# Optimization experiments

Measured on AMD Instinct MI355X. Metric: run time of the kernel, lower is better.

Reference implementation:

```python
import jax, jax.numpy as jnp
import numpy as np

N, E, F, H, A, C, NC, L, AH = 50000, 800000, 768, 256, 128, 128, 7, 2, 4

def _ln(x, g, b):
    m = jnp.mean(x, axis=-1, keepdims=True)
    v = jnp.var(x, axis=-1, keepdims=True)
    return (x - m) / jnp.sqrt(v + 1e-5) * g + b

def setup_inputs() -> dict:
    key = jax.random.key(0)
    ks = jax.random.split(key, 32)
    s = 0.02
    d = {}
    d['x'] = jax.random.normal(ks[0], (N, F), jnp.float32)
    d['edge_index'] = jax.random.randint(ks[1], (2, E), 0, N, jnp.int32)
    d['W_in'] = jax.random.normal(ks[2], (F, H), jnp.float32) * s
    d['b_in'] = jnp.zeros((H,), jnp.float32)
    d['gin_W1'] = jax.random.normal(ks[3], (L, H, H), jnp.float32) * s
    d['gin_b1'] = jnp.zeros((L, H), jnp.float32)
    d['gin_lng'] = jnp.ones((L, H), jnp.float32)
    d['gin_lnb'] = jnp.zeros((L, H), jnp.float32)
    d['gin_W2'] = jax.random.normal(ks[4], (L, H, H), jnp.float32) * s
    d['gin_b2'] = jnp.zeros((L, H), jnp.float32)
    d['eps'] = jnp.zeros((L,), jnp.float32)
    d['ln_g'] = jnp.ones((L, H), jnp.float32)
    d['ln_b'] = jnp.zeros((L, H), jnp.float32)
    d['att_W1'] = jax.random.normal(ks[5], (AH, H, A), jnp.float32) * s
    d['att_b1'] = jnp.zeros((AH, A), jnp.float32)
    d['att_W2'] = jax.random.normal(ks[6], (AH, A), jnp.float32) * s
    d['att_b2'] = jnp.zeros((AH,), jnp.float32)
    d['Wc1'] = jax.random.normal(ks[7], (H, C), jnp.float32) * s
    d['bc1'] = jnp.zeros((C,), jnp.float32)
    d['lnc1_g'] = jnp.ones((C,), jnp.float32)
    d['lnc1_b'] = jnp.zeros((C,), jnp.float32)
    d['Wc2'] = jax.random.normal(ks[8], (C, C // 2), jnp.float32) * s
    d['bc2'] = jnp.zeros((C // 2,), jnp.float32)
    d['lnc2_g'] = jnp.ones((C // 2,), jnp.float32)
    d['lnc2_b'] = jnp.zeros((C // 2,), jnp.float32)
    d['Wc3'] = jax.random.normal(ks[9], (C // 2, NC), jnp.float32) * s
    d['bc3'] = jnp.zeros((NC,), jnp.float32)
    return d

def reference(x, edge_index, W_in, b_in, gin_W1, gin_b1, gin_lng, gin_lnb, gin_W2, gin_b2, eps, ln_g, ln_b, att_W1, att_b1, att_W2, att_b2, Wc1, bc1, lnc1_g, lnc1_b, Wc2, bc2, lnc2_g, lnc2_b, Wc3, bc3):
    src, dst = edge_index[0], edge_index[1]
    # input projection (use_residual and input_dim != gnn_hidden)
    h = x @ W_in + b_in  # [N,H]
    for i in range(L):
        agg = jax.ops.segment_sum(h[src], dst, num_segments=N)  # GIN sum aggregation
        m = (1.0 + eps[i]) * h + agg
        m = _ln(m @ gin_W1[i] + gin_b1[i], gin_lng[i], gin_lnb[i])
        m = jax.nn.relu(m) @ gin_W2[i] + gin_b2[i]
        hn = jax.nn.relu(_ln(m, ln_g[i], ln_b[i]))
        h = hn + h  # residual (shapes match)
    # multi-head attention pooling, softmax over node dim
    s = jnp.tanh(jnp.einsum('nd,kda->kna', h, att_W1) + att_b1[:, None, :])  # [AH,N,A]
    logits = jnp.einsum('kna,ka->kn', s, att_W2) + att_b2[:, None]  # [AH,N]
    a = jax.nn.softmax(logits, axis=1)  # [AH,N]
    z = jnp.einsum('kn,nd->kd', a, h)  # [AH,H]
    z_agg = jnp.mean(z, axis=0)  # [H]
    attn = a.T  # [N,AH]
    # classifier (full variant)
    c = jax.nn.relu(_ln(z_agg @ Wc1 + bc1, lnc1_g, lnc1_b))
    c = jax.nn.relu(_ln(c @ Wc2 + bc2, lnc2_g, lnc2_b))
    probs = jax.nn.softmax(c @ Wc3 + bc3, axis=0)
    return probs, attn
```

## Files before the change

### kernel.cpp

```cpp
#include <hip/hip_runtime.h>
#include <math.h>

#define NN 50000
#define NE 800000
#define FF 768
#define HH 256

typedef __attribute__((ext_vector_type(8))) short short8;
typedef __attribute__((ext_vector_type(4))) float f32x4;

__device__ inline unsigned short f2bf(float f) {
  unsigned u = __float_as_uint(f);
  u = u + 0x7fffu + ((u >> 16) & 1u);
  return (unsigned short)(u >> 16);
}
__device__ inline float bf2f(unsigned short b) {
  return __uint_as_float(((unsigned)b) << 16);
}

__device__ __forceinline__ void ldsload16(const unsigned short* g, unsigned short* l) {
  __builtin_amdgcn_global_load_lds(
      (const __attribute__((address_space(1))) void*)g,
      (__attribute__((address_space(3))) void*)l, 16, 0, 0);
}

__global__ void k_count(const int* __restrict__ dstv, int* __restrict__ deg) {
  int e = blockIdx.x * 256 + threadIdx.x;
  if (e < NE) atomicAdd(&deg[dstv[e]], 1);
}

__global__ void k_scan(const int* __restrict__ deg, int* __restrict__ rowptr) {
  const int CH = 49;
  int tid = threadIdx.x;
  int lane = tid & 63, w = tid >> 6;
  int base = tid * CH;
  int sum = 0;
  for (int i = 0; i < CH; i++) {
    int idx = base + i;
    if (idx < NN) sum += deg[idx];
  }
  int incl = sum;
  for (int off = 1; off < 64; off <<= 1) {
    int tv = __shfl_up(incl, off, 64);
    if (lane >= off) incl += tv;
  }
  __shared__ int ws[16];
  if (lane == 63) ws[w] = incl;
  __syncthreads();
  if (tid == 0) {
    int c = 0;
    for (int i = 0; i < 16; i++) { int tv = ws[i]; ws[i] = c; c += tv; }
  }
  __syncthreads();
  int run = ws[w] + (incl - sum);
  if (tid == 0) rowptr[0] = 0;
  for (int i = 0; i < CH; i++) {
    int idx = base + i;
    if (idx < NN) { run += deg[idx]; rowptr[idx + 1] = run; }
  }
}

__global__ void k_scatter(const int* __restrict__ srcv, const int* __restrict__ dstv,
                          int* __restrict__ cursor, int* __restrict__ csr_src) {
  int e = blockIdx.x * 256 + threadIdx.x;
  if (e < NE) {
    int d = dstv[e];
    int pos = atomicAdd(&cursor[d], 1);
    csr_src[pos] = srcv[e];
  }
}

__global__ void k_agg(const unsigned short* __restrict__ hb, const int* __restrict__ rowptr,
                      const int* __restrict__ csr_src, const float* __restrict__ eps,
                      int layer, unsigned short* __restrict__ mb) {
  int node = (blockIdx.x * blockDim.x + threadIdx.x) >> 6;
  int lane = threadIdx.x & 63;
  if (node >= NN) return;
  int beg = rowptr[node], end = rowptr[node + 1];
  const ushort4* hv = (const ushort4*)hb;
  float ax = 0.f, ay = 0.f, az = 0.f, aw = 0.f;
  int e = beg;
  for (; e + 3 < end; e += 4) {
    int s0 = csr_src[e], s1 = csr_src[e + 1], s2 = csr_src[e + 2], s3 = csr_src[e + 3];
    ushort4 v0 = hv[(size_t)s0 * 64 + lane];
    ushort4 v1 = hv[(size_t)s1 * 64 + lane];
    ushort4 v2 = hv[(size_t)s2 * 64 + lane];
    ushort4 v3 = hv[(size_t)s3 * 64 + lane];
    ax += bf2f(v0.x) + bf2f(v1.x) + bf2f(v2.x) + bf2f(v3.x);
    ay += bf2f(v0.y) + bf2f(v1.y) + bf2f(v2.y) + bf2f(v3.y);
    az += bf2f(v0.z) + bf2f(v1.z) + bf2f(v2.z) + bf2f(v3.z);
    aw += bf2f(v0.w) + bf2f(v1.w) + bf2f(v2.w) + bf2f(v3.w);
  }
  for (; e < end; ++e) {
    int s = csr_src[e];
    ushort4 v = hv[(size_t)s * 64 + lane];
    ax += bf2f(v.x); ay += bf2f(v.y); az += bf2f(v.z); aw += bf2f(v.w);
  }
  float ep = 1.0f + eps[layer];
  ushort4 h0 = hv[(size_t)node * 64 + lane];
  ax += ep * bf2f(h0.x); ay += ep * bf2f(h0.y);
  az += ep * bf2f(h0.z); aw += ep * bf2f(h0.w);
  ushort4 o;
  o.x = f2bf(ax); o.y = f2bf(ay); o.z = f2bf(az); o.w = f2bf(aw);
  *(ushort4*)&mb[(size_t)node * 256 + lane * 4] = o;
}

__global__ void k_tcast(const float* __restrict__ src0, unsigned short* __restrict__ dst0,
                        int R, int C) {
  const float* src = src0 + (size_t)blockIdx.z * R * C;
  unsigned short* dst = dst0 + (size_t)blockIdx.z * R * C;
  __shared__ float tile[32][33];
  int bx = blockIdx.x * 32, by = blockIdx.y * 32;
  int tx = threadIdx.x & 31, ty = threadIdx.x >> 5;
  for (int i = 0; i < 32; i += 8) {
    int r = by + ty + i, c = bx + tx;
    tile[ty + i][tx] = (r < R && c < C) ? src[(size_t)r * C + c] : 0.f;
  }
  __syncthreads();
  for (int i = 0; i < 32; i += 8) {
    int c = bx + ty + i, r = by + tx;
    if (c < C && r < R) dst[(size_t)c * R + r] = f2bf(tile[tx][ty + i]);
  }
}

__global__ __launch_bounds__(256) void k_mmff(
    const float* __restrict__ x, const unsigned short* __restrict__ Bt,
    const float* __restrict__ bias, float* __restrict__ outf,
    unsigned short* __restrict__ outb) {
  __shared__ unsigned short As[64 * 32];
  __shared__ unsigned short Bs[256 * 32];
  int t = threadIdx.x, lane = t & 63, wave = t >> 6;
  int row0 = blockIdx.x * 64;
  f32x4 acc[4][4];
#pragma unroll
  for (int i = 0; i < 4; i++)
#pragma unroll
    for (int j = 0; j < 4; j++) acc[i][j] = (f32x4)(0.f);
  int m16 = lane & 15, kq = lane >> 4;
  int arow = t >> 2, a2 = t & 3;
  int asl = a2 ^ (arow & 3);
  int agr = row0 + arow; if (agr >= NN) agr = NN - 1;
  int brow_[4], bsl_[4];
#pragma unroll
  for (int j = 0; j < 4; j++) {
    int s = j * 256 + t;
    brow_[j] = s >> 2;
    bsl_[j] = (s & 3) ^ (brow_[j] & 3);
  }
  for (int k0 = 0; k0 < FF; k0 += 32) {
    {
      const float* Af = x + (size_t)agr * FF + k0 + asl * 8;
      float4 f0 = *(const float4*)Af;
      float4 f1 = *(const float4*)(Af + 4);
      short8 v;
      v[0] = (short)f2bf(f0.x); v[1] = (short)f2bf(f0.y);
      v[2] = (short)f2bf(f0.z); v[3] = (short)f2bf(f0.w);
      v[4] = (short)f2bf(f1.x); v[5] = (short)f2bf(f1.y);
      v[6] = (short)f2bf(f1.z); v[7] = (short)f2bf(f1.w);
      *(short8*)&As[arow * 32 + a2 * 8] = v;
    }
#pragma unroll
    for (int j = 0; j < 4; j++)
      ldsload16(&Bt[(size_t)brow_[j] * FF + k0 + bsl_[j] * 8],
                &Bs[(j * 256 + wave * 64) * 8]);
    __syncthreads();
    short8 a[4], b[4];
#pragma unroll
    for (int rt = 0; rt < 4; rt++) {
      int row = rt * 16 + m16;
      a[rt] = *(const short8*)&As[row * 32 + ((kq ^ (row & 3)) * 8)];
    }
#pragma unroll
    for (int ct = 0; ct < 4; ct++) {
      int row = wave * 64 + ct * 16 + m16;
      b[ct] = *(const short8*)&Bs[row * 32 + ((kq ^ (row & 3)) * 8)];
    }
#pragma unroll
    for (int rt = 0; rt < 4; rt++)
#pragma unroll
      for (int ct = 0; ct < 4; ct++)
        acc[rt][ct] = __builtin_amdgcn_mfma_f32_16x16x32_bf16(a[rt], b[ct], acc[rt][ct], 0, 0, 0);
    __syncthreads();
  }
  int colbase = wave * 64 + m16;
  float bv[4];
#pragma unroll
  for (int ct = 0; ct < 4; ct++) bv[ct] = bias[colbase + ct * 16];
#pragma unroll
  for (int rt = 0; rt < 4; rt++)
#pragma unroll
    for (int reg = 0; reg < 4; reg++) {
      int r = row0 + rt * 16 + kq * 4 + reg;
      if (r < NN) {
#pragma unroll
        for (int ct = 0; ct < 4; ct++) {
          float v = acc[rt][ct][reg] + bv[ct];
          outf[(size_t)r * 256 + colbase + ct * 16] = v;
          outb[(size_t)r * 256 + colbase + ct * 16] = f2bf(v);
        }
      }
    }
}

template <bool WF, bool ATT>
__global__ __launch_bounds__(256) void k_gin(
    const unsigned short* __restrict__ Ab,
    const unsigned short* __restrict__ B1t, const float* __restrict__ bias1,
    const float* __restrict__ g1v, const float* __restrict__ be1,
    const unsigned short* __restrict__ B2t, const float* __restrict__ bias2,
    const float* __restrict__ g2v, const float* __restrict__ be2,
    const float* __restrict__ resid, float* __restrict__ outf,
    unsigned short* __restrict__ outb,
    const unsigned short* __restrict__ aW1T, const float* __restrict__ ab1,
    const float* __restrict__ aW2v, const float* __restrict__ ab2,
    float* __restrict__ logitsT) {
  __shared__ unsigned short As[2][64 * 32];
  __shared__ unsigned short Bs[2][256 * 32];
  __shared__ unsigned short T1[64 * 256];
  __shared__ float redS[4][64];
  __shared__ float redQ[4][64];
  __shared__ float mvM[64], mvI[64];
  __shared__ float lg[4][64];
  int t = threadIdx.x, lane = t & 63, wave = t >> 6;
  int row0 = blockIdx.x * 64;
  int m16 = lane & 15, kq = lane >> 4;
  int colbase = wave * 64 + m16;
  int arow = t >> 2, a2 = t & 3;
  int asl = a2 ^ (arow & 3);
  int agr = row0 + arow; if (agr >= NN) agr = NN - 1;
  const unsigned short* Ag = Ab + (size_t)agr * 256 + asl * 8;
  int brow_[4], bsl_[4];
#pragma unroll
  for (int j = 0; j < 4; j++) {
    int s = j * 256 + t;
    brow_[j] = s >> 2;
    bsl_[j] = (s & 3) ^ (brow_[j] & 3);
  }
  auto stage1 = [&](int c, int p) {
    int k0 = c * 32;
    ldsload16(Ag + k0, &As[p][wave * 512]);
#pragma unroll
    for (int j = 0; j < 4; j++)
      ldsload16(&B1t[(size_t)brow_[j] * 256 + k0 + bsl_[j] * 8],
                &Bs[p][(j * 256 + wave * 64) * 8]);
  };
  auto stageB = [&](const unsigned short* Bp_, int c, int p) {
    int k0 = c * 32;
#pragma unroll
    for (int j = 0; j < 4; j++)
      ldsload16(&Bp_[(size_t)brow_[j] * 256 + k0 + bsl_[j] * 8],
                &Bs[p][(j * 256 + wave * 64) * 8]);
  };

  f32x4 acc[4][4];
#pragma unroll
  for (int i = 0; i < 4; i++)
#pragma unroll
    for (int j = 0; j < 4; j++) acc[i][j] = (f32x4)(0.f);

  stage1(0, 0);
  stage1(1, 1);
#pragma unroll
  for (int c = 0; c < 8; c++) {
    if (c < 7) asm volatile("s_waitcnt vmcnt(5)" ::: "memory");
    else       asm volatile("s_waitcnt vmcnt(0)" ::: "memory");
    __builtin_amdgcn_s_barrier();
    asm volatile("" ::: "memory");
    const unsigned short* Ap = As[c & 1];
    const unsigned short* Bp = Bs[c & 1];
    short8 a[4], b[4];
#pragma unroll
    for (int rt = 0; rt < 4; rt++) {
      int row = rt * 16 + m16;
      a[rt] = *(const short8*)&Ap[row * 32 + ((kq ^ (row & 3)) * 8)];
    }
#pragma unroll
    for (int ct = 0; ct < 4; ct++) {
      int row = wave * 64 + ct * 16 + m16;
      b[ct] = *(const short8*)&Bp[row * 32 + ((kq ^ (row & 3)) * 8)];
    }
#pragma unroll
    for (int rt = 0; rt < 4; rt++)
#pragma unroll
      for (int ct = 0; ct < 4; ct++)
        acc[rt][ct] = __builtin_amdgcn_mfma_f32_16x16x32_bf16(a[rt], b[ct], acc[rt][ct], 0, 0, 0);
    asm volatile("" ::: "memory");
    __builtin_amdgcn_s_barrier();
    asm volatile("" ::: "memory");
    if (c + 2 < 8) stage1(c + 2, c & 1);
  }

  {
    float bv[4];
#pragma unroll
    for (int ct = 0; ct < 4; ct++) bv[ct] = bias1[colbase + ct * 16];
    float s[4][4], q[4][4];
#pragma unroll
    for (int rt = 0; rt < 4; rt++)
#pragma unroll
      for (int reg = 0; reg < 4; reg++) { s[rt][reg] = 0.f; q[rt][reg] = 0.f; }
#pragma unroll
    for (int rt = 0; rt < 4; rt++)
#pragma unroll
      for (int ct = 0; ct < 4; ct++)
#pragma unroll
        for (int reg = 0; reg < 4; reg++) {
          float v = acc[rt][ct][reg] + bv[ct];
          acc[rt][ct][reg] = v;
          s[rt][reg] += v;
          q[rt][reg] += v * v;
        }
#pragma unroll
    for (int off = 1; off < 16; off <<= 1) {
#pragma unroll
      for (int rt = 0; rt < 4; rt++)
#pragma unroll
        for (int reg = 0; reg < 4; reg++) {
          s[rt][reg] += __shfl_xor(s[rt][reg], off, 64);
          q[rt][reg] += __shfl_xor(q[rt][reg], off, 64);
        }
    }
    if (m16 == 0) {
#pragma unroll
      for (int rt = 0; rt < 4; rt++)
#pragma unroll
        for (int reg = 0; reg < 4; reg++) {
          redS[wave][rt * 16 + kq * 4 + reg] = s[rt][reg];
          redQ[wave][rt * 16 + kq * 4 + reg] = q[rt][reg];
        }
    }
    __syncthreads();
    if (t < 64) {
      float ss = redS[0][t] + redS[1][t] + redS[2][t] + redS[3][t];
      float qq = redQ[0][t] + redQ[1][t] + redQ[2][t] + redQ[3][t];
      float mean = ss * (1.f / 256.f);
      float var = qq * (1.f / 256.f) - mean * mean;
      mvM[t] = mean;
      mvI[t] = rsqrtf(var + 1e-5f);
    }
    __syncthreads();
    float gv[4], bev[4];
#pragma unroll
    for (int ct = 0; ct < 4; ct++) { gv[ct] = g1v[colbase + ct * 16]; bev[ct] = be1[colbase + ct * 16]; }
#pragma unroll
    for (int rt = 0; rt < 4; rt++)
#pragma unroll
      for (int reg = 0; reg < 4; reg++) {
        int rr = rt * 16 + kq * 4 + reg;
        float mean = mvM[rr], inv = mvI[rr];
#pragma unroll
        for (int ct = 0; ct < 4; ct++) {
          int col = colbase + ct * 16;
          float val = fmaxf((acc[rt][ct][reg] - mean) * inv * gv[ct] + bev[ct], 0.f);
          T1[rr * 256 + (((col >> 3) ^ (rr & 31)) * 8) + (col & 7)] = f2bf(val);
        }
      }
    __syncthreads();
  }

#pragma unroll
  for (int i = 0; i < 4; i++)
#pragma unroll
    for (int j = 0; j < 4; j++) acc[i][j] = (f32x4)(0.f);
  stageB(B2t, 0, 0);
  stageB(B2t, 1, 1);
#pragma unroll
  for (int c = 0; c < 8; c++) {
    if (c < 7) asm volatile("s_waitcnt vmcnt(4)" ::: "memory");
    else       asm volatile("s_waitcnt vmcnt(0)" ::: "memory");
    __builtin_amdgcn_s_barrier();
    asm volatile("" ::: "memory");
    const unsigned short* Bp = Bs[c & 1];
    short8 a[4], b[4];
#pragma unroll
    for (int rt = 0; rt < 4; rt++) {
      int row = rt * 16 + m16;
      int sl = (c * 4 + kq) ^ (row & 31);
      a[rt] = *(const short8*)&T1[row * 256 + sl * 8];
    }
#pragma unroll
    for (int ct = 0; ct < 4; ct++) {
      int row = wave * 64 + ct * 16 + m16;
      b[ct] = *(const short8*)&Bp[row * 32 + ((kq ^ (row & 3)) * 8)];
    }
#pragma unroll
    for (int rt = 0; rt < 4; rt++)
#pragma unroll
      for (int ct = 0; ct < 4; ct++)
        acc[rt][ct] = __builtin_amdgcn_mfma_f32_16x16x32_bf16(a[rt], b[ct], acc[rt][ct], 0, 0, 0);
    asm volatile("" ::: "memory");
    __builtin_amdgcn_s_barrier();
    asm volatile("" ::: "memory");
    if (c + 2 < 8) stageB(B2t, c + 2, c & 1);
  }

  {
    float bv[4];
#pragma unroll
    for (int ct = 0; ct < 4; ct++) bv[ct] = bias2[colbase + ct * 16];
    float s[4][4], q[4][4];
#pragma unroll
    for (int rt = 0; rt < 4; rt++)
#pragma unroll
      for (int reg = 0; reg < 4; reg++) { s[rt][reg] = 0.f; q[rt][reg] = 0.f; }
#pragma unroll
    for (int rt = 0; rt < 4; rt++)
#pragma unroll
      for (int ct = 0; ct < 4; ct++)
#pragma unroll
        for (int reg = 0; reg < 4; reg++) {
          float v = acc[rt][ct][reg] + bv[ct];
          acc[rt][ct][reg] = v;
          s[rt][reg] += v;
          q[rt][reg] += v * v;
        }
#pragma unroll
    for (int off = 1; off < 16; off <<= 1) {
#pragma unroll
      for (int rt = 0; rt < 4; rt++)
#pragma unroll
        for (int reg = 0; reg < 4; reg++) {
          s[rt][reg] += __shfl_xor(s[rt][reg], off, 64);
          q[rt][reg] += __shfl_xor(q[rt][reg], off, 64);
        }
    }
    if (m16 == 0) {
#pragma unroll
      for (int rt = 0; rt < 4; rt++)
#pragma unroll
        for (int reg = 0; reg < 4; reg++) {
          redS[wave][rt * 16 + kq * 4 + reg] = s[rt][reg];
          redQ[wave][rt * 16 + kq * 4 + reg] = q[rt][reg];
        }
    }
    __syncthreads();
    if (t < 64) {
      float ss = redS[0][t] + redS[1][t] + redS[2][t] + redS[3][t];
      float qq = redQ[0][t] + redQ[1][t] + redQ[2][t] + redQ[3][t];
      float mean = ss * (1.f / 256.f);
      float var = qq * (1.f / 256.f) - mean * mean;
      mvM[t] = mean;
      mvI[t] = rsqrtf(var + 1e-5f);
    }
    __syncthreads();
    float gv[4], bev[4];
#pragma unroll
    for (int ct = 0; ct < 4; ct++) { gv[ct] = g2v[colbase + ct * 16]; bev[ct] = be2[colbase + ct * 16]; }
#pragma unroll
    for (int rt = 0; rt < 4; rt++)
#pragma unroll
      for (int reg = 0; reg < 4; reg++) {
        int rr = rt * 16 + kq * 4 + reg;
        int r = row0 + rr;
        if (r >= NN) continue;
        float mean = mvM[rr], inv = mvI[rr];
#pragma unroll
        for (int ct = 0; ct < 4; ct++) {
          int col = colbase + ct * 16;
          float val = fmaxf((acc[rt][ct][reg] - mean) * inv * gv[ct] + bev[ct], 0.f);
          val += resid[(size_t)r * 256 + col];
          if (WF) outf[(size_t)r * 256 + col] = val;
          outb[(size_t)r * 256 + col] = f2bf(val);
          if (ATT) T1[rr * 256 + (((col >> 3) ^ (rr & 31)) * 8) + (col & 7)] = f2bf(val);
        }
      }
  }

  if (ATT) {
    ((float*)lg)[t] = 0.f;
    __syncthreads();
#pragma unroll
    for (int pass = 0; pass < 2; pass++) {
#pragma unroll
      for (int i = 0; i < 4; i++)
#pragma unroll
        for (int j = 0; j < 4; j++) acc[i][j] = (f32x4)(0.f);
      const unsigned short* Wp = aW1T + (size_t)pass * 256 * 256;
      stageB(Wp, 0, 0);
      stageB(Wp, 1, 1);
#pragma unroll
      for (int c = 0; c < 8; c++) {
        if (c < 7) asm volatile("s_waitcnt vmcnt(4)" ::: "memory");
        else       asm volatile("s_waitcnt vmcnt(0)" ::: "memory");
        __builtin_amdgcn_s_barrier();
        asm volatile("" ::: "memory");
        const unsigned short* Bp = Bs[c & 1];
        short8 a[4], b[4];
#pragma unroll
        for (int rt = 0; rt < 4; rt++) {
          int row = rt * 16 + m16;
          int sl = (c * 4 + kq) ^ (row & 31);
          a[rt] = *(const short8*)&T1[row * 256 + sl * 8];
        }
#pragma unroll
        for (int ct = 0; ct < 4; ct++) {
          int row = wave * 64 + ct * 16 + m16;
          b[ct] = *(const short8*)&Bp[row * 32 + ((kq ^ (row & 3)) * 8)];
        }
#pragma unroll
        for (int rt = 0; rt < 4; rt++)
#pragma unroll
          for (int ct = 0; ct < 4; ct++)
            acc[rt][ct] = __builtin_amdgcn_mfma_f32_16x16x32_bf16(a[rt], b[ct], acc[rt][ct], 0, 0, 0);
        asm volatile("" ::: "memory");
        __builtin_amdgcn_s_barrier();
        asm volatile("" ::: "memory");
        if (c + 2 < 8) stageB(Wp, c + 2, c & 1);
      }
      int head = pass * 2 + (wave >> 1);
      const float* b1k = ab1 + head * 128;
      const float* w2k = aW2v + head * 128;
      float p[4][4];
#pragma unroll
      for (int rt = 0; rt < 4; rt++)
#pragma unroll
        for (int reg = 0; reg < 4; reg++) p[rt][reg] = 0.f;
#pragma unroll
      for (int ct = 0; ct < 4; ct++) {
        int hcol = (wave & 1) * 64 + ct * 16 + m16;
        float b1v = b1k[hcol], w2v = w2k[hcol];
#pragma unroll
        for (int rt = 0; rt < 4; rt++)
#pragma unroll
          for (int reg = 0; reg < 4; reg++) {
            float xv = acc[rt][ct][reg] + b1v;
            xv = fminf(fmaxf(xv, -10.f), 10.f);
            float ex = __expf(2.f * xv);
            p[rt][reg] += (ex - 1.f) / (ex + 1.f) * w2v;
          }
      }
#pragma unroll
      for (int off = 1; off < 16; off <<= 1)
#pragma unroll
        for (int rt = 0; rt < 4; rt++)
#pragma unroll
          for (int reg = 0; reg < 4; reg++) p[rt][reg] += __shfl_xor(p[rt][reg], off, 64);
      if (m16 == 0) {
#pragma unroll
        for (int rt = 0; rt < 4; rt++)
#pragma unroll
          for (int reg = 0; reg < 4; reg++)
            atomicAdd(&lg[head][rt * 16 + kq * 4 + reg], p[rt][reg]);
      }
    }
    __syncthreads();
    int hh = t >> 6, rr2 = t & 63;
    int r = row0 + rr2;
    if (r < NN) logitsT[(size_t)hh * NN + r] = lg[hh][rr2] + ab2[hh];
  }
}

__global__ void k_smax1(const float* __restrict__ logitsT, float* __restrict__ pmax,
                        float* __restrict__ psum) {
  int k = blockIdx.y;
  int tid = threadIdx.x;
  const float* L = logitsT + (size_t)k * NN;
  __shared__ float sm[256];
  float mx = -1e30f;
  for (int i = blockIdx.x * 256 + tid; i < NN; i += 128 * 256) mx = fmaxf(mx, L[i]);
  sm[tid] = mx; __syncthreads();
  for (int o = 128; o >= 1; o >>= 1) { if (tid < o) sm[tid] = fmaxf(sm[tid], sm[tid + o]); __syncthreads(); }
  float bmax = sm[0];
  __syncthreads();
  float s = 0.f;
  for (int i = blockIdx.x * 256 + tid; i < NN; i += 128 * 256) s += __expf(L[i] - bmax);
  sm[tid] = s; __syncthreads();
  for (int o = 128; o >= 1; o >>= 1) { if (tid < o) sm[tid] += sm[tid + o]; __syncthreads(); }
  if (tid == 0) { pmax[k * 128 + blockIdx.x] = bmax; psum[k * 128 + blockIdx.x] = sm[0]; }
}

__global__ void k_smax2(const float* __restrict__ pmax, const float* __restrict__ psum,
                        float* __restrict__ gs) {
  int k = blockIdx.x;
  int tid = threadIdx.x;
  __shared__ float sm[128], sv[128];
  float m = pmax[k * 128 + tid];
  sm[tid] = m; __syncthreads();
  for (int o = 64; o >= 1; o >>= 1) { if (tid < o) sm[tid] = fmaxf(sm[tid], sm[tid + o]); __syncthreads(); }
  float gm = sm[0];
  __syncthreads();
  sv[tid] = psum[k * 128 + tid] * __expf(m - gm);
  __syncthreads();
  for (int o = 64; o >= 1; o >>= 1) { if (tid < o) sv[tid] += sv[tid + o]; __syncthreads(); }
  if (tid == 0) { gs[k * 2] = gm; gs[k * 2 + 1] = sv[0]; }
}

__global__ void k_attnz(const float* __restrict__ logitsT, const float* __restrict__ gs,
                        const unsigned short* __restrict__ hb, float* __restrict__ out_attn,
                        float* __restrict__ z) {
  int n0 = blockIdx.x * 128;
  int tid = threadIdx.x;
  __shared__ float a[4][128];
  for (int i = tid; i < 512; i += 256) {
    int k = i >> 7, n = i & 127;
    float v = 0.f;
    if (n0 + n < NN) v = __expf(logitsT[(size_t)k * NN + n0 + n] - gs[k * 2]) / gs[k * 2 + 1];
    a[k][n] = v;
  }
  __syncthreads();
  for (int i = tid; i < 512; i += 256) {
    int n = i >> 2, k = i & 3;
    if (n0 + n < NN) out_attn[(size_t)(n0 + n) * 4 + k] = a[k][n];
  }
  float z0 = 0.f, z1 = 0.f, z2 = 0.f, z3 = 0.f;
  int d = tid;
  int nmax = NN - n0; if (nmax > 128) nmax = 128;
  for (int n = 0; n < nmax; n++) {
    float hv = bf2f(hb[(size_t)(n0 + n) * 256 + d]);
    z0 += a[0][n] * hv; z1 += a[1][n] * hv; z2 += a[2][n] * hv; z3 += a[3][n] * hv;
  }
  atomicAdd(&z[0 * 256 + d], z0);
  atomicAdd(&z[1 * 256 + d], z1);
  atomicAdd(&z[2 * 256 + d], z2);
  atomicAdd(&z[3 * 256 + d], z3);
}

__global__ void k_cls(const float* __restrict__ z, const float* __restrict__ Wc1,
                      const float* __restrict__ bc1, const float* __restrict__ g1,
                      const float* __restrict__ b1, const float* __restrict__ Wc2,
                      const float* __restrict__ bc2, const float* __restrict__ g2,
                      const float* __restrict__ b2, const float* __restrict__ Wc3,
                      const float* __restrict__ bc3, float* __restrict__ out) {
  int tid = threadIdx.x;
  __shared__ float za[256];
  __shared__ float buf[256];
  __shared__ float c1s[128];
  __shared__ float c2s[64];
  za[tid] = 0.25f * (z[tid] + z[256 + tid] + z[512 + tid] + z[768 + tid]);
  __syncthreads();
  float v1 = 0.f;
  if (tid < 128) {
    for (int d = 0; d < 256; d++) v1 += za[d] * Wc1[d * 128 + tid];
    v1 += bc1[tid];
  }
  buf[tid] = (tid < 128) ? v1 : 0.f; __syncthreads();
  for (int o = 128; o >= 1; o >>= 1) { if (tid < o) buf[tid] += buf[tid + o]; __syncthreads(); }
  float mean1 = buf[0] * (1.f / 128.f);
  __syncthreads();
  buf[tid] = (tid < 128) ? (v1 - mean1) * (v1 - mean1) : 0.f; __syncthreads();
  for (int o = 128; o >= 1; o >>= 1) { if (tid < o) buf[tid] += buf[tid + o]; __syncthreads(); }
  float inv1 = rsqrtf(buf[0] * (1.f / 128.f) + 1e-5f);
  __syncthreads();
  if (tid < 128) c1s[tid] = fmaxf((v1 - mean1) * inv1 * g1[tid] + b1[tid], 0.f);
  __syncthreads();
  float v2 = 0.f;
  if (tid < 64) {
    for (int d = 0; d < 128; d++) v2 += c1s[d] * Wc2[d * 64 + tid];
    v2 += bc2[tid];
  }
  buf[tid] = (tid < 64) ? v2 : 0.f; __syncthreads();
  for (int o = 128; o >= 1; o >>= 1) { if (tid < o) buf[tid] += buf[tid + o]; __syncthreads(); }
  float mean2 = buf[0] * (1.f / 64.f);
  __syncthreads();
  buf[tid] = (tid < 64) ? (v2 - mean2) * (v2 - mean2) : 0.f; __syncthreads();
  for (int o = 128; o >= 1; o >>= 1) { if (tid < o) buf[tid] += buf[tid + o]; __syncthreads(); }
  float inv2 = rsqrtf(buf[0] * (1.f / 64.f) + 1e-5f);
  __syncthreads();
  if (tid < 64) c2s[tid] = fmaxf((v2 - mean2) * inv2 * g2[tid] + b2[tid], 0.f);
  __syncthreads();
  if (tid < 7) {
    float l = 0.f;
    for (int d = 0; d < 64; d++) l += c2s[d] * Wc3[d * 7 + tid];
    buf[tid] = l + bc3[tid];
  }
  __syncthreads();
  if (tid == 0) {
    float mx = -1e30f;
    for (int i = 0; i < 7; i++) mx = fmaxf(mx, buf[i]);
    float s = 0.f;
    for (int i = 0; i < 7; i++) s += __expf(buf[i] - mx);
    for (int i = 0; i < 7; i++) out[i] = __expf(buf[i] - mx) / s;
  }
}

extern "C" void kernel_launch(void* const* d_in, const int* in_sizes, int n_in,
                              void* d_out, int out_size, void* d_ws, size_t ws_size,
                              hipStream_t stream) {
  const float* x       = (const float*)d_in[0];
  const int*   ei      = (const int*)d_in[1];
  const float* W_in    = (const float*)d_in[2];
  const float* b_in    = (const float*)d_in[3];
  const float* gin_W1  = (const float*)d_in[4];
  const float* gin_b1  = (const float*)d_in[5];
  const float* gin_lng = (const float*)d_in[6];
  const float* gin_lnb = (const float*)d_in[7];
  const float* gin_W2  = (const float*)d_in[8];
  const float* gin_b2  = (const float*)d_in[9];
  const float* eps     = (const float*)d_in[10];
  const float* ln_g    = (const float*)d_in[11];
  const float* ln_b    = (const float*)d_in[12];
  const float* att_W1  = (const float*)d_in[13];
  const float* att_b1  = (const float*)d_in[14];
  const float* att_W2  = (const float*)d_in[15];
  const float* att_b2  = (const float*)d_in[16];
  const float* Wc1     = (const float*)d_in[17];
  const float* bc1     = (const float*)d_in[18];
  const float* lnc1_g  = (const float*)d_in[19];
  const float* lnc1_b  = (const float*)d_in[20];
  const float* Wc2     = (const float*)d_in[21];
  const float* bc2     = (const float*)d_in[22];
  const float* lnc2_g  = (const float*)d_in[23];
  const float* lnc2_b  = (const float*)d_in[24];
  const float* Wc3     = (const float*)d_in[25];
  const float* bc3     = (const float*)d_in[26];
  float* out = (float*)d_out;
  (void)in_sizes; (void)n_in; (void)out_size; (void)ws_size;

  char* wsb = (char*)d_ws;
  size_t off = 0;
  auto alloc = [&](size_t bytes) {
    char* p = wsb + off;
    off += (bytes + 255) & ~(size_t)255;
    return p;
  };
  float*          h       = (float*)alloc((size_t)NN * HH * 4);
  unsigned short* hb      = (unsigned short*)alloc((size_t)NN * HH * 2);
  unsigned short* mb1     = (unsigned short*)alloc((size_t)NN * HH * 2);
  unsigned short* WinT    = (unsigned short*)alloc((size_t)HH * FF * 2);
  unsigned short* g1T     = (unsigned short*)alloc((size_t)2 * HH * HH * 2);
  unsigned short* g2T     = (unsigned short*)alloc((size_t)2 * HH * HH * 2);
  unsigned short* aW1T    = (unsigned short*)alloc((size_t)4 * 128 * HH * 2);
  float*          logitsT = (float*)alloc((size_t)4 * NN * 4);
  int*            deg     = (int*)alloc((size_t)NN * 4);
  int*            rowptr  = (int*)alloc((size_t)(NN + 1) * 4);
  int*            cursor  = (int*)alloc((size_t)NN * 4);
  int*            csr_src = (int*)alloc((size_t)NE * 4);
  float*          pmax    = (float*)alloc(4 * 128 * 4);
  float*          psum    = (float*)alloc(4 * 128 * 4);
  float*          gs      = (float*)alloc(8 * 4);
  float*          z       = (float*)alloc(4 * 256 * 4);

  const int* srcv = ei;
  const int* dstv = ei + NE;

  k_tcast<<<dim3((HH + 31) / 32, (FF + 31) / 32, 1), 256, 0, stream>>>(W_in, WinT, FF, HH);
  k_tcast<<<dim3(8, 8, 2), 256, 0, stream>>>(gin_W1, g1T, HH, HH);
  k_tcast<<<dim3(8, 8, 2), 256, 0, stream>>>(gin_W2, g2T, HH, HH);
  k_tcast<<<dim3(4, 8, 4), 256, 0, stream>>>(att_W1, aW1T, HH, 128);

  hipMemsetAsync(deg, 0, (size_t)NN * 4, stream);
  hipMemsetAsync(z, 0, 4 * 256 * 4, stream);
  k_count<<<(NE + 255) / 256, 256, 0, stream>>>(dstv, deg);
  k_scan<<<1, 1024, 0, stream>>>(deg, rowptr);
  hipMemcpyAsync(cursor, rowptr, (size_t)NN * 4, hipMemcpyDeviceToDevice, stream);
  k_scatter<<<(NE + 255) / 256, 256, 0, stream>>>(srcv, dstv, cursor, csr_src);

  int gblocks = (NN + 63) / 64;
  k_mmff<<<gblocks, 256, 0, stream>>>(x, WinT, b_in, h, hb);

  for (int l = 0; l < 2; l++) {
    k_agg<<<(NN + 3) / 4, 256, 0, stream>>>(hb, rowptr, csr_src, eps, l, mb1);
    if (l == 0)
      k_gin<true, false><<<gblocks, 256, 0, stream>>>(
          mb1, g1T + (size_t)l * HH * HH, gin_b1 + l * HH, gin_lng + l * HH, gin_lnb + l * HH,
          g2T + (size_t)l * HH * HH, gin_b2 + l * HH, ln_g + l * HH, ln_b + l * HH,
          h, h, hb, nullptr, nullptr, nullptr, nullptr, nullptr);
    else
      k_gin<false, true><<<gblocks, 256, 0, stream>>>(
          mb1, g1T + (size_t)l * HH * HH, gin_b1 + l * HH, gin_lng + l * HH, gin_lnb + l * HH,
          g2T + (size_t)l * HH * HH, gin_b2 + l * HH, ln_g + l * HH, ln_b + l * HH,
          h, nullptr, hb, aW1T, att_b1, att_W2, att_b2, logitsT);
  }

  k_smax1<<<dim3(128, 4), 256, 0, stream>>>(logitsT, pmax, psum);
  k_smax2<<<4, 128, 0, stream>>>(pmax, psum, gs);
  k_attnz<<<(NN + 127) / 128, 256, 0, stream>>>(logitsT, gs, hb, out + 7, z);
  k_cls<<<1, 256, 0, stream>>>(z, Wc1, bc1, lnc1_g, lnc1_b, Wc2, bc2, lnc2_g, lnc2_b,
                               Wc3, bc3, out);
}
```

Before: 874.9 us.

## Compute attention scores in one pass with per-wave heads

Replaces the two-pass attention-score GEMM, where each wave held half a head, with a single pass. Each wave now owns one full head (128 columns) and keeps 4x8 accumulators, so logits are written directly without the shared-memory atomic reduction buffer. The B tile is loaded as a single 512x32 buffer spanning both Bs halves, with a barrier before and after each K chunk, so the old double-buffered prefetch is gone. This doubles accumulator registers, which risks lower occupancy or spills, and load latency is no longer overlapped.

```diff
diff --git a/kernel.cpp b/kernel.cpp
--- a/kernel.cpp
+++ b/kernel.cpp
@@ -220,7 +220,6 @@
   __shared__ float redS[4][64];
   __shared__ float redQ[4][64];
   __shared__ float mvM[64], mvI[64];
-  __shared__ float lg[4][64];
   int t = threadIdx.x, lane = t & 63, wave = t >> 6;
   int row0 = blockIdx.x * 64;
   int m16 = lane & 15, kq = lane >> 4;
@@ -467,86 +466,81 @@
   }
 
   if (ATT) {
-    ((float*)lg)[t] = 0.f;
     __syncthreads();
-#pragma unroll
-    for (int pass = 0; pass < 2; pass++) {
-#pragma unroll
-      for (int i = 0; i < 4; i++)
-#pragma unroll
-        for (int j = 0; j < 4; j++) acc[i][j] = (f32x4)(0.f);
-      const unsigned short* Wp = aW1T + (size_t)pass * 256 * 256;
-      stageB(Wp, 0, 0);
-      stageB(Wp, 1, 1);
-#pragma unroll
-      for (int c = 0; c < 8; c++) {
-        if (c < 7) asm volatile("s_waitcnt vmcnt(4)" ::: "memory");
-        else       asm volatile("s_waitcnt vmcnt(0)" ::: "memory");
-        __builtin_amdgcn_s_barrier();
-        asm volatile("" ::: "memory");
-        const unsigned short* Bp = Bs[c & 1];
-        short8 a[4], b[4];
-#pragma unroll
-        for (int rt = 0; rt < 4; rt++) {
-          int row = rt * 16 + m16;
-          int sl = (c * 4 + kq) ^ (row & 31);
-          a[rt] = *(const short8*)&T1[row * 256 + sl * 8];
-        }
-#pragma unroll
-        for (int ct = 0; ct < 4; ct++) {
-          int row = wave * 64 + ct * 16 + m16;
-          b[ct] = *(const short8*)&Bp[row * 32 + ((kq ^ (row & 3)) * 8)];
-        }
+    f32x4 acc8[4][8];
+#pragma unroll
+    for (int i = 0; i < 4; i++)
+#pragma unroll
+      for (int j = 0; j < 8; j++) acc8[i][j] = (f32x4)(0.f);
+    unsigned short* BsU = &Bs[0][0];
+    int brow8_[8], bsl8_[8];
+#pragma unroll
+    for (int j = 0; j < 8; j++) {
+      int s = j * 256 + t;
+      brow8_[j] = s >> 2;
+      bsl8_[j] = (s & 3) ^ (brow8_[j] & 3);
+    }
+#pragma unroll
+    for (int c = 0; c < 8; c++) {
+#pragma unroll
+      for (int j = 0; j < 8; j++)
+        ldsload16(&aW1T[(size_t)brow8_[j] * 256 + c * 32 + bsl8_[j] * 8],
+                  &BsU[(j * 256 + wave * 64) * 8]);
+      __syncthreads();
+      short8 a[4];
+#pragma unroll
+      for (int rt = 0; rt < 4; rt++) {
+        int row = rt * 16 + m16;
+        int sl = (c * 4 + kq) ^ (row & 31);
+        a[rt] = *(const short8*)&T1[row * 256 + sl * 8];
+      }
+#pragma unroll
+      for (int ct = 0; ct < 8; ct++) {
+        int row = wave * 128 + ct * 16 + m16;
+        short8 b = *(const short8*)&BsU[row * 32 + ((kq ^ (row & 3)) * 8)];
 #pragma unroll
         for (int rt = 0; rt < 4; rt++)
-#pragma unroll
-          for (int ct = 0; ct < 4; ct++)
-            acc[rt][ct] = __builtin_amdgcn_mfma_f32_16x16x32_bf16(a[rt], b[ct], acc[rt][ct], 0, 0, 0);
-        asm volatile("" ::: "memory");
-        __builtin_amdgcn_s_barrier();
-        asm volatile("" ::: "memory");
-        if (c + 2 < 8) stageB(Wp, c + 2, c & 1);
+          acc8[rt][ct] = __builtin_amdgcn_mfma_f32_16x16x32_bf16(a[rt], b, acc8[rt][ct], 0, 0, 0);
       }
-      int head = pass * 2 + (wave >> 1);
-      const float* b1k = ab1 + head * 128;
-      const float* w2k = aW2v + head * 128;
-      float p[4][4];
+      __syncthreads();
+    }
+    const float* b1k = ab1 + wave * 128;
+    const float* w2k = aW2v + wave * 128;
+    float p[4][4];
+#pragma unroll
+    for (int rt = 0; rt < 4; rt++)
+#pragma unroll
+      for (int reg = 0; reg < 4; reg++) p[rt][reg] = 0.f;
+#pragma unroll
+    for (int ct = 0; ct < 8; ct++) {
+      int col = ct * 16 + m16;
+      float b1v = b1k[col], w2v = w2k[col];
 #pragma unroll
       for (int rt = 0; rt < 4; rt++)
 #pragma unroll
-        for (int reg = 0; reg < 4; reg++) p[rt][reg] = 0.f;
-#pragma unroll
-      for (int ct = 0; ct < 4; ct++) {
-        int hcol = (wave & 1) * 64 + ct * 16 + m16;
-        float b1v = b1k[hcol], w2v = w2k[hcol];
-#pragma unroll
-        for (int rt = 0; rt < 4; rt++)
-#pragma unroll
-          for (int reg = 0; reg < 4; reg++) {
-            float xv = acc[rt][ct][reg] + b1v;
-            xv = fminf(fmaxf(xv, -10.f), 10.f);
-            float ex = __expf(2.f * xv);
-            p[rt][reg] += (ex - 1.f) / (ex + 1.f) * w2v;
-          }
-      }
-#pragma unroll
-      for (int off = 1; off < 16; off <<= 1)
-#pragma unroll
-        for (int rt = 0; rt < 4; rt++)
-#pragma unroll
-          for (int reg = 0; reg < 4; reg++) p[rt][reg] += __shfl_xor(p[rt][reg], off, 64);
-      if (m16 == 0) {
-#pragma unroll
-        for (int rt = 0; rt < 4; rt++)
-#pragma unroll
-          for (int reg = 0; reg < 4; reg++)
-            atomicAdd(&lg[head][rt * 16 + kq * 4 + reg], p[rt][reg]);
-      }
-    }
-    __syncthreads();
-    int hh = t >> 6, rr2 = t & 63;
-    int r = row0 + rr2;
-    if (r < NN) logitsT[(size_t)hh * NN + r] = lg[hh][rr2] + ab2[hh];
+        for (int reg = 0; reg < 4; reg++) {
+          float xv = acc8[rt][ct][reg] + b1v;
+          xv = fminf(fmaxf(xv, -10.f), 10.f);
+          float ex = __expf(2.f * xv);
+          p[rt][reg] += (ex - 1.f) / (ex + 1.f) * w2v;
+        }
+    }
+#pragma unroll
+    for (int off = 1; off < 16; off <<= 1)
+#pragma unroll
+      for (int rt = 0; rt < 4; rt++)
+#pragma unroll
+        for (int reg = 0; reg < 4; reg++) p[rt][reg] += __shfl_xor(p[rt][reg], off, 64);
+    if (m16 == 0) {
+      float b2v = ab2[wave];
+#pragma unroll
+      for (int rt = 0; rt < 4; rt++)
+#pragma unroll
+        for (int reg = 0; reg < 4; reg++) {
+          int r = row0 + rt * 16 + kq * 4 + reg;
+          if (r < NN) logitsT[(size_t)wave * NN + r] = p[rt][reg] + b2v;
+        }
+    }
   }
 }
 
```

New measurement: 987.5 us. 12.9% more time.
